# Kernel optimization log

Measured on AMD Instinct MI355X. Metric: run time of the kernel, lower is better.

The kernel has to match this reference:

```python
import jax, jax.numpy as jnp
import numpy as np

NUM_HEADS = 16
DIM = 1024


def setup_inputs() -> dict:
    key = jax.random.key(0)
    k1, k2, k3, k4 = jax.random.split(key, 4)
    B, N, C = 4, 2048, DIM
    x = jax.random.normal(k1, (B, N, C), dtype=jnp.float32)
    # weights stored in apply orientation: y = x @ W (+ b)
    W_qkv = jax.random.normal(k2, (C, 3 * C), dtype=jnp.float32) * (C ** -0.5)
    W_out = jax.random.normal(k3, (C, C), dtype=jnp.float32) * (C ** -0.5)
    b_out = jax.random.normal(k4, (C,), dtype=jnp.float32) * 0.01
    return {"hidden_states": x, "W_qkv": W_qkv, "W_out": W_out, "b_out": b_out}


def reference(hidden_states, W_qkv, W_out, b_out):
    B, N, C = hidden_states.shape
    H = NUM_HEADS
    Dh = C // H
    scale = Dh ** -0.5
    qkv = hidden_states @ W_qkv                      # [B, N, 3C]
    qkv = qkv.reshape(B, N, 3, H, Dh).transpose(2, 0, 3, 1, 4)  # [3, B, H, N, Dh]
    q, k, v = qkv[0], qkv[1], qkv[2]
    scores = jnp.einsum('bhnd,bhmd->bhnm', q, k) * scale  # [B, H, N, N]
    probs = jax.nn.softmax(scores, axis=-1)
    out = jnp.einsum('bhnm,bhmd->bhnd', probs, v)    # [B, H, N, Dh]
    out = out.transpose(0, 2, 1, 3).reshape(B, N, C)  # merge heads
    return out @ W_out + b_out                        # dropout p=0 -> identity
```

## Files before the change

kernel.cpp:

```cpp
#include <hip/hip_runtime.h>
#include <hip/hip_bf16.h>
#include <stdint.h>

#define BATCH 4
#define SEQN  2048
#define DIMC  1024
#define NHEADS 16
#define DHEAD 64
#define BH_TOT 64
#define MROWS 8192

typedef __attribute__((ext_vector_type(8))) short bf16x8;
typedef __attribute__((ext_vector_type(4))) float f32x4;

__device__ __forceinline__ unsigned short bf16_rtne(float f){
  union { float f; unsigned u; } v; v.f = f;
  unsigned u = v.u;
  return (unsigned short)((u + 0x7FFFu + ((u >> 16) & 1u)) >> 16);
}
__device__ __forceinline__ float bf16f(unsigned short h){
  union { unsigned u; float f; } v; v.u = ((unsigned)h) << 16;
  return v.f;
}
__device__ __forceinline__ unsigned cvt_pk_bf16(float lo, float hi){
  unsigned r;
  asm("v_cvt_pk_bf16_f32 %0, %1, %2" : "=v"(r) : "v"(lo), "v"(hi));
  return r;
}

__device__ __forceinline__ void async16(void* lds, const void* g){
  __builtin_amdgcn_global_load_lds((const __attribute__((address_space(1))) void*)g,
                                   (__attribute__((address_space(3))) void*)lds, 16, 0, 0);
}

__global__ __launch_bounds__(256) void split_rows_k(const float* __restrict__ X,
    unsigned short* __restrict__ O, int nrows, int Kc){
  int q4 = Kc >> 2;
  int total = nrows * q4;
  int idx = blockIdx.x*256 + threadIdx.x;
  if (idx >= total) return;
  int row = idx / q4, c = idx - row*q4;
  const float4 v = *(const float4*)(X + ((size_t)row*Kc + c*4));
  float fv[4] = {v.x, v.y, v.z, v.w};
  unsigned short hi[4], lo[4];
#pragma unroll
  for (int j=0;j<4;j++){ hi[j] = bf16_rtne(fv[j]); lo[j] = bf16_rtne(fv[j] - bf16f(hi[j])); }
  size_t ob = (size_t)row*(2*Kc) + c*4;
  ushort4 h; h.x=hi[0]; h.y=hi[1]; h.z=hi[2]; h.w=hi[3];
  ushort4 l2; l2.x=lo[0]; l2.y=lo[1]; l2.z=lo[2]; l2.w=lo[3];
  *(ushort4*)(O + ob) = h;
  *(ushort4*)(O + ob + Kc) = l2;
}

__global__ __launch_bounds__(256) void transpose_split_k(const float* __restrict__ W,
    unsigned short* __restrict__ Wt, int K, int Nc){
  __shared__ float tile[32][33];
  int tx = threadIdx.x & 31, ty = threadIdx.x >> 5;
  int n0 = blockIdx.x*32, k0 = blockIdx.y*32;
#pragma unroll
  for (int i=0;i<4;i++){
    int k = k0 + ty + i*8;
    tile[ty + i*8][tx] = W[(size_t)k*Nc + n0 + tx];
  }
  __syncthreads();
#pragma unroll
  for (int i=0;i<4;i++){
    int n = n0 + ty + i*8;
    float f = tile[tx][ty + i*8];
    unsigned short hi = bf16_rtne(f);
    unsigned short lo = bf16_rtne(f - bf16f(hi));
    Wt[(size_t)n*(2*K) + k0 + tx] = hi;
    Wt[(size_t)n*(2*K) + K + k0 + tx] = lo;
  }
}

__global__ __launch_bounds__(256) void gemm_split_k(
    const unsigned short* __restrict__ A, const unsigned short* __restrict__ Bt,
    float* __restrict__ C, const float* __restrict__ bias, int M, int Nc, int K)
{
  __shared__ unsigned short a_lds[2][4096];
  __shared__ unsigned short b_lds[2][4096];
  const int t = threadIdx.x, w = t>>6, l = t&63, lg = l>>4, ll = l&15;
  const int wr = w>>1, wc = w&1;
  const int nbx = gridDim.x;
  const int nwg = nbx * gridDim.y;
  const int orig = blockIdx.y*nbx + blockIdx.x;
  const int id = ((orig & 7) * (nwg >> 3)) + (orig >> 3);
  const int m0 = (id % nbx)*128, n0 = (id / nbx)*128;
  const int ldk = 2*K;
  const int nkt = (3*K) >> 5;
  f32x4 acc[4][4];
#pragma unroll
  for (int m=0;m<4;m++)
#pragma unroll
    for (int n=0;n<4;n++) acc[m][n] = (f32x4){0.f,0.f,0.f,0.f};

  auto stage = [&](int buf, int kt){
    int kp = kt*32;
    int ac = (kp < K)   ? kp : kp - K;
    int bc = (kp < 2*K) ? kp : kp - 2*K;
#pragma unroll
    for (int i=0;i<2;i++){
      int s = t + i*256; int row = s>>2; int sl = s&3; int sl2 = sl ^ (row&3);
      async16(&a_lds[buf][s*8], A + (size_t)(m0+row)*ldk + ac + sl2*8);
    }
#pragma unroll
    for (int i=0;i<2;i++){
      int s = t + i*256; int row = s>>2; int sl = s&3; int sl2 = sl ^ (row&3);
      async16(&b_lds[buf][s*8], Bt + (size_t)(n0+row)*ldk + bc + sl2*8);
    }
  };

  stage(0, 0);
  __syncthreads();
  for (int kt=0; kt<nkt; ++kt){
    int cur = kt&1;
    if (kt+1 < nkt) stage(cur^1, kt+1);
    bf16x8 af[4], bfr[4];
#pragma unroll
    for (int m=0;m<4;m++){
      int row = wr*64 + m*16 + ll;
      af[m] = *(const bf16x8*)&a_lds[cur][row*32 + ((lg ^ (row&3))*8)];
    }
#pragma unroll
    for (int n=0;n<4;n++){
      int row = wc*64 + n*16 + ll;
      bfr[n] = *(const bf16x8*)&b_lds[cur][row*32 + ((lg ^ (row&3))*8)];
    }
#pragma unroll
    for (int m=0;m<4;m++)
#pragma unroll
      for (int n=0;n<4;n++)
        acc[m][n] = __builtin_amdgcn_mfma_f32_16x16x32_bf16(af[m], bfr[n], acc[m][n], 0,0,0);
    __syncthreads();
  }
#pragma unroll
  for (int m=0;m<4;m++)
#pragma unroll
    for (int n=0;n<4;n++){
      int col = n0 + wc*64 + n*16 + ll;
      float bv = bias ? bias[col] : 0.f;
#pragma unroll
      for (int r=0;r<4;r++){
        int row = m0 + wr*64 + m*16 + lg*4 + r;
        C[(size_t)row*Nc + col] = acc[m][n][r] + bv;
      }
    }
}

#define QSCALE 0.18033688f
__global__ __launch_bounds__(256) void split_qk_k(const float* __restrict__ qkv,
    unsigned short* __restrict__ Qo, unsigned short* __restrict__ Ko){
  int idx = blockIdx.x*256 + threadIdx.x;
  int d4 = idx & 15, n = (idx>>4) & (SEQN-1), bh = idx >> 15;
  int b = bh>>4, h = bh&15;
  size_t base = ((size_t)(b*SEQN + n))*3072 + h*64 + d4*4;
  float4 q = *(const float4*)(qkv + base);
  float4 k = *(const float4*)(qkv + base + 1024);
  float fq[4] = {q.x*QSCALE, q.y*QSCALE, q.z*QSCALE, q.w*QSCALE};
  float fk[4] = {k.x, k.y, k.z, k.w};
  unsigned short qh[4], ql[4], kh[4];
#pragma unroll
  for (int j=0;j<4;j++){
    qh[j] = bf16_rtne(fq[j]); ql[j] = bf16_rtne(fq[j] - bf16f(qh[j]));
    kh[j] = bf16_rtne(fk[j]);
  }
  size_t obq = ((size_t)bh*SEQN + n)*128 + d4*4;
  size_t obk = ((size_t)bh*SEQN + n)*64 + d4*4;
  ushort4 u;
  u.x=qh[0];u.y=qh[1];u.z=qh[2];u.w=qh[3]; *(ushort4*)(Qo+obq) = u;
  u.x=ql[0];u.y=ql[1];u.z=ql[2];u.w=ql[3]; *(ushort4*)(Qo+obq+64) = u;
  u.x=kh[0];u.y=kh[1];u.z=kh[2];u.w=kh[3]; *(ushort4*)(Ko+obk) = u;
}

__global__ __launch_bounds__(256) void build_vt_k(const float* __restrict__ qkv,
    unsigned short* __restrict__ Vt){
  __shared__ float tile[64][65];
  const int mt = blockIdx.x, bh = blockIdx.y;
  const int b = bh>>4, h = bh&15;
  const int t = threadIdx.x;
  const int r = t>>2, seg = t&3;
  size_t src = ((size_t)(b*SEQN + mt*64 + r))*3072 + 2048 + h*64 + seg*16;
#pragma unroll
  for (int j=0;j<4;j++){
    float4 v = *(const float4*)(qkv + src + j*4);
    tile[r][seg*16 + j*4 + 0] = v.x;
    tile[r][seg*16 + j*4 + 1] = v.y;
    tile[r][seg*16 + j*4 + 2] = v.z;
    tile[r][seg*16 + j*4 + 3] = v.w;
  }
  __syncthreads();
  const int d = r, ms = seg;
  unsigned short o16[16];
#pragma unroll
  for (int j=0;j<16;j++) o16[j] = bf16_rtne(tile[ms*16 + j][d]);
  size_t dst = ((size_t)(bh*64 + d))*SEQN + mt*64 + ms*16;
  uint4 u0, u1;
  unsigned* pu = (unsigned*)&u0;
  unsigned* pv = (unsigned*)&u1;
#pragma unroll
  for (int j=0;j<4;j++){
    pu[j] = (unsigned)o16[2*j]   | ((unsigned)o16[2*j+1]<<16);
    pv[j] = (unsigned)o16[8+2*j] | ((unsigned)o16[9+2*j]<<16);
  }
  *(uint4*)(Vt + dst) = u0;
  *(uint4*)(Vt + dst + 8) = u1;
}

__global__ __launch_bounds__(256, 4) void attn_k(const unsigned short* __restrict__ Q,
    const unsigned short* __restrict__ Kh, const unsigned short* __restrict__ Vt,
    float* __restrict__ att)
{
  __shared__ unsigned short k_lds[2][4096];
  __shared__ unsigned short v_lds[2][4096];
  __shared__ unsigned p_lds[4][512];
  const int orig = blockIdx.y*gridDim.x + blockIdx.x;
  const int id = ((orig & 7) << 8) + (orig >> 3);
  const int qt = id & 31, bh = id >> 5;
  const int b = bh>>4, h = bh&15;
  const int t = threadIdx.x, w = t>>6, l = t&63, lg = l>>4, ll = l&15;
  const size_t kvbase = (size_t)bh*SEQN;

  bf16x8 qf[4];
  {
    size_t qrow = (kvbase + qt*64 + w*16 + ll) * 128;
#pragma unroll
    for (int i=0;i<4;i++)
      qf[i] = *(const bf16x8*)(Q + qrow + i*32 + lg*8);
  }
  f32x4 o[4];
#pragma unroll
  for (int d=0; d<4; d++) o[d] = (f32x4){0.f,0.f,0.f,0.f};
  float lsum = 0.f;

  auto stage = [&](int buf, int kv){
    int m0 = kv*64;
#pragma unroll
    for (int i=0;i<2;i++){
      int s = t + i*256; int row = s>>3; int sl = s&7; int sl2 = sl ^ (row&7);
      async16(&k_lds[buf][s*8], Kh + (kvbase + m0 + row)*64 + sl2*8);
    }
#pragma unroll
    for (int i=0;i<2;i++){
      int s = t + i*256; int row = s>>3; int sl = s&7; int sl2 = sl ^ (row&7);
      async16(&v_lds[buf][s*8], Vt + ((size_t)bh*64 + row)*SEQN + m0 + sl2*8);
    }
  };

  stage(0, 0);
  __syncthreads();
  const int NKV = SEQN/64;
  for (int kv=0; kv<NKV; ++kv){
    int cur = kv&1;
    if (kv+1 < NKV) stage(cur^1, kv+1);
#pragma unroll
    for (int nt=0; nt<4; ++nt){
      int row = nt*16 + ll;
      bf16x8 kf0 = *(const bf16x8*)&k_lds[cur][row*64 + (((0*4+lg) ^ (row&7))*8)];
      bf16x8 kf1 = *(const bf16x8*)&k_lds[cur][row*64 + (((1*4+lg) ^ (row&7))*8)];
      f32x4 a = (f32x4){0.f,0.f,0.f,0.f};
      __builtin_amdgcn_s_setprio(1);
      a = __builtin_amdgcn_mfma_f32_16x16x32_bf16(kf0, qf[0], a, 0,0,0);
      a = __builtin_amdgcn_mfma_f32_16x16x32_bf16(kf1, qf[1], a, 0,0,0);
      a = __builtin_amdgcn_mfma_f32_16x16x32_bf16(kf0, qf[2], a, 0,0,0);
      a = __builtin_amdgcn_mfma_f32_16x16x32_bf16(kf1, qf[3], a, 0,0,0);
      __builtin_amdgcn_s_setprio(0);
      float e0 = exp2f(a[0]), e1 = exp2f(a[1]), e2 = exp2f(a[2]), e3 = exp2f(a[3]);
      lsum += (e0 + e1) + (e2 + e3);
      unsigned pk0 = cvt_pk_bf16(e0, e1);
      unsigned pk1 = cvt_pk_bf16(e2, e3);
      int c0 = nt*8 + lg*2;
      int addr = ll*32 + (((c0>>2) ^ (ll&7))<<2) + (c0&3);
      *(uint2*)&p_lds[w][addr] = make_uint2(pk0, pk1);
    }
#pragma unroll
    for (int ks=0; ks<2; ++ks){
      int chunk = ks*4 + lg;
      bf16x8 pf = *(const bf16x8*)&p_lds[w][ll*32 + ((chunk ^ (ll&7))<<2)];
      __builtin_amdgcn_s_setprio(1);
#pragma unroll
      for (int dt=0; dt<4; ++dt){
        int row = dt*16 + ll;
        bf16x8 vf = *(const bf16x8*)&v_lds[cur][row*64 + (((ks*4+lg) ^ (row&7))*8)];
        o[dt] = __builtin_amdgcn_mfma_f32_16x16x32_bf16(pf, vf, o[dt], 0,0,0);
      }
      __builtin_amdgcn_s_setprio(0);
    }
    __syncthreads();
  }
  float tot = lsum;
  tot += __shfl_xor(tot, 16);
  tot += __shfl_xor(tot, 32);
  float inv = 1.0f / tot;
#pragma unroll
  for (int r=0;r<4;r++){
    float rl = __shfl(inv, lg*4 + r);
    int qrow = qt*64 + w*16 + lg*4 + r;
    size_t ob = ((size_t)(b*SEQN + qrow))*DIMC + h*64;
#pragma unroll
    for (int dt=0; dt<4; ++dt)
      att[ob + dt*16 + ll] = o[dt][r] * rl;
  }
}

extern "C" void kernel_launch(void* const* d_in, const int* in_sizes, int n_in,
                              void* d_out, int out_size, void* d_ws, size_t ws_size,
                              hipStream_t stream){
  const float* x    = (const float*)d_in[0];
  const float* Wqkv = (const float*)d_in[1];
  const float* Wout = (const float*)d_in[2];
  const float* bout = (const float*)d_in[3];
  float* out = (float*)d_out;

  char* ws = (char*)d_ws;
  size_t off = 0;
  auto walloc = [&](size_t bytes) -> void* {
    void* p = ws + off; off += (bytes + 255) & ~(size_t)255; return p;
  };
  unsigned short* x_hl   = (unsigned short*)walloc((size_t)MROWS*2048*2);
  unsigned short* wqkv_t = (unsigned short*)walloc((size_t)3072*2048*2);
  float*          qkv    = (float*)walloc((size_t)MROWS*3072*4);
  unsigned short* q_hl   = (unsigned short*)walloc((size_t)BH_TOT*SEQN*128*2);
  unsigned short* k_h    = (unsigned short*)walloc((size_t)BH_TOT*SEQN*64*2);
  unsigned short* vt     = (unsigned short*)walloc((size_t)BH_TOT*64*SEQN*2);
  unsigned short* wout_t = (unsigned short*)walloc((size_t)1024*2048*2);
  float*          att    = qkv;
  unsigned short* att_hl = x_hl;

  split_rows_k<<<8192, 256, 0, stream>>>(x, x_hl, MROWS, DIMC);
  transpose_split_k<<<dim3(3072/32, 1024/32), 256, 0, stream>>>(Wqkv, wqkv_t, 1024, 3072);
  transpose_split_k<<<dim3(1024/32, 1024/32), 256, 0, stream>>>(Wout, wout_t, 1024, 1024);
  gemm_split_k<<<dim3(MROWS/128, 3072/128), 256, 0, stream>>>(x_hl, wqkv_t, qkv, nullptr, MROWS, 3072, 1024);
  split_qk_k<<<(BH_TOT*SEQN*16)/256, 256, 0, stream>>>(qkv, q_hl, k_h);
  build_vt_k<<<dim3(SEQN/64, BH_TOT), 256, 0, stream>>>(qkv, vt);
  attn_k<<<dim3(SEQN/64, BH_TOT), 256, 0, stream>>>(q_hl, k_h, vt, att);
  split_rows_k<<<8192, 256, 0, stream>>>(att, att_hl, MROWS, DIMC);
  gemm_split_k<<<dim3(MROWS/128, 1024/128), 256, 0, stream>>>(att_hl, wout_t, out, bout, MROWS, 1024, 1024);
}
```

Baseline: 545.8 us.

## Deepen GEMM k-tile pipeline with fragment-ordered LDS and fuse attention output split

The split-bf16 GEMM now stages 64-wide k tiles as two 32-wide halves stored in MFMA fragment order, so no XOR swizzle is needed. Each half is double-buffered and loaded with explicit vmcnt waits and raw barriers, and the next tile's loads are issued right after the LDS reads so they overlap the MFMAs. The launch moves to a 1D grid with 2 blocks per CU. Separately, the attention kernel writes the hi/lo bf16 split of its output directly, which removes the fp32 intermediate and the extra split_rows pass before the output projection. The cost is double the LDS use per block and fragile hand-written wait counts.

```diff
diff --git a/kernel.cpp b/kernel.cpp
--- a/kernel.cpp
+++ b/kernel.cpp
@@ -74,76 +74,107 @@
   }
 }
 
-__global__ __launch_bounds__(256) void gemm_split_k(
+__global__ __launch_bounds__(256, 2) void gemm_split_k(
     const unsigned short* __restrict__ A, const unsigned short* __restrict__ Bt,
     float* __restrict__ C, const float* __restrict__ bias, int M, int Nc, int K)
 {
-  __shared__ unsigned short a_lds[2][4096];
-  __shared__ unsigned short b_lds[2][4096];
+  __shared__ unsigned short a_lds[2][2][4096];
+  __shared__ unsigned short b_lds[2][2][4096];
   const int t = threadIdx.x, w = t>>6, l = t&63, lg = l>>4, ll = l&15;
   const int wr = w>>1, wc = w&1;
-  const int nbx = gridDim.x;
-  const int nwg = nbx * gridDim.y;
-  const int orig = blockIdx.y*nbx + blockIdx.x;
-  const int id = ((orig & 7) * (nwg >> 3)) + (orig >> 3);
-  const int m0 = (id % nbx)*128, n0 = (id / nbx)*128;
+  const int nbm = M>>7;
+  const int nwg = nbm*(Nc>>7);
+  const int orig = blockIdx.x;
+  const int id = ((orig&7)*(nwg>>3)) + (orig>>3);
+  const int m0 = (id & (nbm-1))<<7, n0 = (id/nbm)<<7;
   const int ldk = 2*K;
-  const int nkt = (3*K) >> 5;
+  const int nkt = (3*K)>>6;
   f32x4 acc[4][4];
 #pragma unroll
   for (int m=0;m<4;m++)
 #pragma unroll
     for (int n=0;n<4;n++) acc[m][n] = (f32x4){0.f,0.f,0.f,0.f};
 
-  auto stage = [&](int buf, int kt){
-    int kp = kt*32;
-    int ac = (kp < K)   ? kp : kp - K;
-    int bc = (kp < 2*K) ? kp : kp - 2*K;
+  auto stage = [&](int d, int kk, int kt){
+    const int kp = kt<<6;
+    const int ac = (kp <   K) ? kp : kp -   K;
+    const int bc = (kp < 2*K) ? kp : kp - 2*K;
 #pragma unroll
     for (int i=0;i<2;i++){
-      int s = t + i*256; int row = s>>2; int sl = s&3; int sl2 = sl ^ (row&3);
-      async16(&a_lds[buf][s*8], A + (size_t)(m0+row)*ldk + ac + sl2*8);
+      int F = i*4 + w;
+      async16(&a_lds[d][kk][(i*256+t)*8],
+              A + (size_t)(m0 + F*16 + ll)*ldk + ac + kk*32 + lg*8);
     }
 #pragma unroll
     for (int i=0;i<2;i++){
-      int s = t + i*256; int row = s>>2; int sl = s&3; int sl2 = sl ^ (row&3);
-      async16(&b_lds[buf][s*8], Bt + (size_t)(n0+row)*ldk + bc + sl2*8);
+      int F = i*4 + w;
+      async16(&b_lds[d][kk][(i*256+t)*8],
+              Bt + (size_t)(n0 + F*16 + ll)*ldk + bc + kk*32 + lg*8);
     }
   };
 
-  stage(0, 0);
-  __syncthreads();
-  for (int kt=0; kt<nkt; ++kt){
-    int cur = kt&1;
-    if (kt+1 < nkt) stage(cur^1, kt+1);
-    bf16x8 af[4], bfr[4];
-#pragma unroll
-    for (int m=0;m<4;m++){
-      int row = wr*64 + m*16 + ll;
-      af[m] = *(const bf16x8*)&a_lds[cur][row*32 + ((lg ^ (row&3))*8)];
-    }
-#pragma unroll
-    for (int n=0;n<4;n++){
-      int row = wc*64 + n*16 + ll;
-      bfr[n] = *(const bf16x8*)&b_lds[cur][row*32 + ((lg ^ (row&3))*8)];
-    }
-#pragma unroll
-    for (int m=0;m<4;m++)
-#pragma unroll
-      for (int n=0;n<4;n++)
-        acc[m][n] = __builtin_amdgcn_mfma_f32_16x16x32_bf16(af[m], bfr[n], acc[m][n], 0,0,0);
-    __syncthreads();
-  }
-#pragma unroll
-  for (int m=0;m<4;m++)
-#pragma unroll
-    for (int n=0;n<4;n++){
-      int col = n0 + wc*64 + n*16 + ll;
+  stage(0, 0, 0);
+  stage(0, 1, 0);
+
+  for (int kt=0; kt<nkt-1; ++kt){
+    const int d = kt&1;
+#pragma unroll
+    for (int kk=0; kk<2; ++kk){
+      asm volatile("s_waitcnt vmcnt(4)" ::: "memory");
+      __builtin_amdgcn_s_barrier();
+      __builtin_amdgcn_sched_barrier(0);
+      bf16x8 af[4], bfr[4];
+#pragma unroll
+      for (int fm=0;fm<4;fm++)
+        af[fm] = *(const bf16x8*)&a_lds[d][kk][(wr*4+fm)*512 + l*8];
+#pragma unroll
+      for (int fn=0;fn<4;fn++)
+        bfr[fn] = *(const bf16x8*)&b_lds[d][kk][(wc*4+fn)*512 + l*8];
+      stage(d^1, kk, kt+1);
+      __builtin_amdgcn_s_setprio(1);
+#pragma unroll
+      for (int fm=0;fm<4;fm++)
+#pragma unroll
+        for (int fn=0;fn<4;fn++)
+          acc[fm][fn] = __builtin_amdgcn_mfma_f32_16x16x32_bf16(af[fm], bfr[fn], acc[fm][fn], 0,0,0);
+      __builtin_amdgcn_s_setprio(0);
+    }
+  }
+  {
+    const int d = (nkt-1)&1;
+#pragma unroll
+    for (int kk=0; kk<2; ++kk){
+      if (kk==0) asm volatile("s_waitcnt vmcnt(4)" ::: "memory");
+      else       asm volatile("s_waitcnt vmcnt(0)" ::: "memory");
+      __builtin_amdgcn_s_barrier();
+      __builtin_amdgcn_sched_barrier(0);
+      bf16x8 af[4], bfr[4];
+#pragma unroll
+      for (int fm=0;fm<4;fm++)
+        af[fm] = *(const bf16x8*)&a_lds[d][kk][(wr*4+fm)*512 + l*8];
+#pragma unroll
+      for (int fn=0;fn<4;fn++)
+        bfr[fn] = *(const bf16x8*)&b_lds[d][kk][(wc*4+fn)*512 + l*8];
+      __builtin_amdgcn_s_setprio(1);
+#pragma unroll
+      for (int fm=0;fm<4;fm++)
+#pragma unroll
+        for (int fn=0;fn<4;fn++)
+          acc[fm][fn] = __builtin_amdgcn_mfma_f32_16x16x32_bf16(af[fm], bfr[fn], acc[fm][fn], 0,0,0);
+      __builtin_amdgcn_s_setprio(0);
+    }
+  }
+
+#pragma unroll
+  for (int fm=0;fm<4;fm++)
+#pragma unroll
+    for (int fn=0;fn<4;fn++){
+      int col = n0 + wc*64 + fn*16 + ll;
       float bv = bias ? bias[col] : 0.f;
 #pragma unroll
       for (int r=0;r<4;r++){
-        int row = m0 + wr*64 + m*16 + lg*4 + r;
-        C[(size_t)row*Nc + col] = acc[m][n][r] + bv;
+        int row = m0 + wr*64 + fm*16 + lg*4 + r;
+        C[(size_t)row*Nc + col] = acc[fm][fn][r] + bv;
       }
     }
 }
@@ -209,7 +240,7 @@
 
 __global__ __launch_bounds__(256, 4) void attn_k(const unsigned short* __restrict__ Q,
     const unsigned short* __restrict__ Kh, const unsigned short* __restrict__ Vt,
-    float* __restrict__ att)
+    unsigned short* __restrict__ att_hl)
 {
   __shared__ unsigned short k_lds[2][4096];
   __shared__ unsigned short v_lds[2][4096];
@@ -296,10 +327,15 @@
   for (int r=0;r<4;r++){
     float rl = __shfl(inv, lg*4 + r);
     int qrow = qt*64 + w*16 + lg*4 + r;
-    size_t ob = ((size_t)(b*SEQN + qrow))*DIMC + h*64;
-#pragma unroll
-    for (int dt=0; dt<4; ++dt)
-      att[ob + dt*16 + ll] = o[dt][r] * rl;
+    size_t ob = ((size_t)(b*SEQN + qrow))*2048 + h*64;
+#pragma unroll
+    for (int dt=0; dt<4; ++dt){
+      float f = o[dt][r] * rl;
+      unsigned short hi = bf16_rtne(f);
+      unsigned short lo = bf16_rtne(f - bf16f(hi));
+      att_hl[ob + dt*16 + ll] = hi;
+      att_hl[ob + 1024 + dt*16 + ll] = lo;
+    }
   }
 }
 
@@ -324,16 +360,14 @@
   unsigned short* k_h    = (unsigned short*)walloc((size_t)BH_TOT*SEQN*64*2);
   unsigned short* vt     = (unsigned short*)walloc((size_t)BH_TOT*64*SEQN*2);
   unsigned short* wout_t = (unsigned short*)walloc((size_t)1024*2048*2);
-  float*          att    = qkv;
   unsigned short* att_hl = x_hl;
 
   split_rows_k<<<8192, 256, 0, stream>>>(x, x_hl, MROWS, DIMC);
   transpose_split_k<<<dim3(3072/32, 1024/32), 256, 0, stream>>>(Wqkv, wqkv_t, 1024, 3072);
   transpose_split_k<<<dim3(1024/32, 1024/32), 256, 0, stream>>>(Wout, wout_t, 1024, 1024);
-  gemm_split_k<<<dim3(MROWS/128, 3072/128), 256, 0, stream>>>(x_hl, wqkv_t, qkv, nullptr, MROWS, 3072, 1024);
+  gemm_split_k<<<1536, 256, 0, stream>>>(x_hl, wqkv_t, qkv, nullptr, MROWS, 3072, 1024);
   split_qk_k<<<(BH_TOT*SEQN*16)/256, 256, 0, stream>>>(qkv, q_hl, k_h);
   build_vt_k<<<dim3(SEQN/64, BH_TOT), 256, 0, stream>>>(qkv, vt);
-  attn_k<<<dim3(SEQN/64, BH_TOT), 256, 0, stream>>>(q_hl, k_h, vt, att);
-  split_rows_k<<<8192, 256, 0, stream>>>(att, att_hl, MROWS, DIMC);
-  gemm_split_k<<<dim3(MROWS/128, 1024/128), 256, 0, stream>>>(att_hl, wout_t, out, bout, MROWS, 1024, 1024);
-}
+  attn_k<<<dim3(SEQN/64, BH_TOT), 256, 0, stream>>>(q_hl, k_h, vt, att_hl);
+  gemm_split_k<<<512, 256, 0, stream>>>(att_hl, wout_t, out, bout, MROWS, 1024, 1024);
+}
```

After: 629.3 us. 1.15x slower.

## Retile split-bf16 GEMM to 256x128 with triple-buffered LDS; fuse att split

Applied to the files above, without the earlier changes.

The split-bf16 GEMM moves to 512-thread blocks computing 256x128 tiles. It gains a three-stage LDS ring with raw vmcnt waits and one barrier per k-step, MFMA-friendly pre-permuted LDS layout, and setprio around the MFMA loop. The attention kernel now writes the hi/lo bf16 split of its output directly, removing the fp32 att buffer round trip and the separate split_rows launch. Risks are the larger LDS footprint limiting occupancy and correctness depending on the hand-written vmcnt counts.

```diff
diff --git a/kernel.cpp b/kernel.cpp
--- a/kernel.cpp
+++ b/kernel.cpp
@@ -74,76 +74,81 @@
   }
 }
 
-__global__ __launch_bounds__(256) void gemm_split_k(
+__global__ __launch_bounds__(512, 4) void gemm_split_k(
     const unsigned short* __restrict__ A, const unsigned short* __restrict__ Bt,
     float* __restrict__ C, const float* __restrict__ bias, int M, int Nc, int K)
 {
-  __shared__ unsigned short a_lds[2][4096];
-  __shared__ unsigned short b_lds[2][4096];
-  const int t = threadIdx.x, w = t>>6, l = t&63, lg = l>>4, ll = l&15;
-  const int wr = w>>1, wc = w&1;
-  const int nbx = gridDim.x;
-  const int nwg = nbx * gridDim.y;
-  const int orig = blockIdx.y*nbx + blockIdx.x;
-  const int id = ((orig & 7) * (nwg >> 3)) + (orig >> 3);
-  const int m0 = (id % nbx)*128, n0 = (id / nbx)*128;
+  __shared__ unsigned short a_lds[3*8192];
+  __shared__ unsigned short b_lds[3*4096];
+  const int t = threadIdx.x, wid = t>>6, l = t&63, lg = l>>4, ll = l&15;
+  const int wm = wid>>1, wn = wid&1;
+  const int nbm = M>>8;
+  const int nwg = nbm*(Nc>>7);
+  const int orig = blockIdx.x;
+  const int id = ((orig&7)*(nwg>>3)) + (orig>>3);
+  const int m0 = (id % nbm)<<8, n0 = (id / nbm)<<7;
   const int ldk = 2*K;
-  const int nkt = (3*K) >> 5;
+  const int nkt = (3*K)>>5;
   f32x4 acc[4][4];
 #pragma unroll
-  for (int m=0;m<4;m++)
-#pragma unroll
-    for (int n=0;n<4;n++) acc[m][n] = (f32x4){0.f,0.f,0.f,0.f};
-
-  auto stage = [&](int buf, int kt){
-    int kp = kt*32;
-    int ac = (kp < K)   ? kp : kp - K;
-    int bc = (kp < 2*K) ? kp : kp - 2*K;
+  for (int i=0;i<4;i++)
+#pragma unroll
+    for (int j=0;j<4;j++) acc[i][j] = (f32x4){0.f,0.f,0.f,0.f};
+
+  auto stageA = [&](int wb, int kt2){
+    const int kp = kt2<<5;
+    const int ac = (kp < K) ? kp : kp - K;
 #pragma unroll
     for (int i=0;i<2;i++){
-      int s = t + i*256; int row = s>>2; int sl = s&3; int sl2 = sl ^ (row&3);
-      async16(&a_lds[buf][s*8], A + (size_t)(m0+row)*ldk + ac + sl2*8);
-    }
-#pragma unroll
-    for (int i=0;i<2;i++){
-      int s = t + i*256; int row = s>>2; int sl = s&3; int sl2 = sl ^ (row&3);
-      async16(&b_lds[buf][s*8], Bt + (size_t)(n0+row)*ldk + bc + sl2*8);
+      int b = i*8 + wid;
+      async16(&a_lds[wb*8192 + b*512 + l*8],
+              A + (size_t)(m0 + b*16 + ll)*ldk + ac + lg*8);
     }
   };
-
-  stage(0, 0);
-  __syncthreads();
+  auto stageB = [&](int wb, int kt2){
+    const int kp = kt2<<5;
+    const int bc = (kp < 2*K) ? kp : kp - 2*K;
+    async16(&b_lds[wb*4096 + wid*512 + l*8],
+            Bt + (size_t)(n0 + wid*16 + ll)*ldk + bc + lg*8);
+  };
+
+  stageA(0, 0); stageB(0, 0);
+  stageA(1, 1); stageB(1, 1);
+
   for (int kt=0; kt<nkt; ++kt){
-    int cur = kt&1;
-    if (kt+1 < nkt) stage(cur^1, kt+1);
-    bf16x8 af[4], bfr[4];
-#pragma unroll
-    for (int m=0;m<4;m++){
-      int row = wr*64 + m*16 + ll;
-      af[m] = *(const bf16x8*)&a_lds[cur][row*32 + ((lg ^ (row&3))*8)];
-    }
-#pragma unroll
-    for (int n=0;n<4;n++){
-      int row = wc*64 + n*16 + ll;
-      bfr[n] = *(const bf16x8*)&b_lds[cur][row*32 + ((lg ^ (row&3))*8)];
-    }
-#pragma unroll
-    for (int m=0;m<4;m++)
-#pragma unroll
-      for (int n=0;n<4;n++)
-        acc[m][n] = __builtin_amdgcn_mfma_f32_16x16x32_bf16(af[m], bfr[n], acc[m][n], 0,0,0);
-    __syncthreads();
-  }
-#pragma unroll
-  for (int m=0;m<4;m++)
-#pragma unroll
-    for (int n=0;n<4;n++){
-      int col = n0 + wc*64 + n*16 + ll;
+    if (kt < nkt-1) asm volatile("s_waitcnt vmcnt(3)\n\ts_barrier" ::: "memory");
+    else            asm volatile("s_waitcnt vmcnt(0)\n\ts_barrier" ::: "memory");
+    const int rb = kt % 3;
+    const unsigned short* ab = &a_lds[rb*8192];
+    const unsigned short* bb = &b_lds[rb*4096];
+    bf16x8 af[4], bf[4];
+#pragma unroll
+    for (int i=0;i<4;i++) af[i] = *(const bf16x8*)&ab[(wm*4+i)*512 + l*8];
+#pragma unroll
+    for (int j=0;j<4;j++) bf[j] = *(const bf16x8*)&bb[(wn*4+j)*512 + l*8];
+    if (kt+2 < nkt){
+      const int wb = (kt+2) % 3;
+      stageA(wb, kt+2); stageB(wb, kt+2);
+    }
+    __builtin_amdgcn_s_setprio(1);
+#pragma unroll
+    for (int i=0;i<4;i++)
+#pragma unroll
+      for (int j=0;j<4;j++)
+        acc[i][j] = __builtin_amdgcn_mfma_f32_16x16x32_bf16(af[i], bf[j], acc[i][j], 0,0,0);
+    __builtin_amdgcn_s_setprio(0);
+  }
+
+#pragma unroll
+  for (int i=0;i<4;i++)
+#pragma unroll
+    for (int j=0;j<4;j++){
+      int col = n0 + wn*64 + j*16 + ll;
       float bv = bias ? bias[col] : 0.f;
 #pragma unroll
       for (int r=0;r<4;r++){
-        int row = m0 + wr*64 + m*16 + lg*4 + r;
-        C[(size_t)row*Nc + col] = acc[m][n][r] + bv;
+        int row = m0 + wm*64 + i*16 + lg*4 + r;
+        C[(size_t)row*Nc + col] = acc[i][j][r] + bv;
       }
     }
 }
@@ -209,7 +214,7 @@
 
 __global__ __launch_bounds__(256, 4) void attn_k(const unsigned short* __restrict__ Q,
     const unsigned short* __restrict__ Kh, const unsigned short* __restrict__ Vt,
-    float* __restrict__ att)
+    unsigned short* __restrict__ att_hl)
 {
   __shared__ unsigned short k_lds[2][4096];
   __shared__ unsigned short v_lds[2][4096];
@@ -296,10 +301,15 @@
   for (int r=0;r<4;r++){
     float rl = __shfl(inv, lg*4 + r);
     int qrow = qt*64 + w*16 + lg*4 + r;
-    size_t ob = ((size_t)(b*SEQN + qrow))*DIMC + h*64;
-#pragma unroll
-    for (int dt=0; dt<4; ++dt)
-      att[ob + dt*16 + ll] = o[dt][r] * rl;
+    size_t ob = ((size_t)(b*SEQN + qrow))*2048 + h*64;
+#pragma unroll
+    for (int dt=0; dt<4; ++dt){
+      float f = o[dt][r] * rl;
+      unsigned short hi = bf16_rtne(f);
+      unsigned short lo = bf16_rtne(f - bf16f(hi));
+      att_hl[ob + dt*16 + ll] = hi;
+      att_hl[ob + 1024 + dt*16 + ll] = lo;
+    }
   }
 }
 
@@ -324,16 +334,14 @@
   unsigned short* k_h    = (unsigned short*)walloc((size_t)BH_TOT*SEQN*64*2);
   unsigned short* vt     = (unsigned short*)walloc((size_t)BH_TOT*64*SEQN*2);
   unsigned short* wout_t = (unsigned short*)walloc((size_t)1024*2048*2);
-  float*          att    = qkv;
   unsigned short* att_hl = x_hl;
 
   split_rows_k<<<8192, 256, 0, stream>>>(x, x_hl, MROWS, DIMC);
   transpose_split_k<<<dim3(3072/32, 1024/32), 256, 0, stream>>>(Wqkv, wqkv_t, 1024, 3072);
   transpose_split_k<<<dim3(1024/32, 1024/32), 256, 0, stream>>>(Wout, wout_t, 1024, 1024);
-  gemm_split_k<<<dim3(MROWS/128, 3072/128), 256, 0, stream>>>(x_hl, wqkv_t, qkv, nullptr, MROWS, 3072, 1024);
+  gemm_split_k<<<768, 512, 0, stream>>>(x_hl, wqkv_t, qkv, nullptr, MROWS, 3072, 1024);
   split_qk_k<<<(BH_TOT*SEQN*16)/256, 256, 0, stream>>>(qkv, q_hl, k_h);
   build_vt_k<<<dim3(SEQN/64, BH_TOT), 256, 0, stream>>>(qkv, vt);
-  attn_k<<<dim3(SEQN/64, BH_TOT), 256, 0, stream>>>(q_hl, k_h, vt, att);
-  split_rows_k<<<8192, 256, 0, stream>>>(att, att_hl, MROWS, DIMC);
-  gemm_split_k<<<dim3(MROWS/128, 1024/128), 256, 0, stream>>>(att_hl, wout_t, out, bout, MROWS, 1024, 1024);
-}
+  attn_k<<<dim3(SEQN/64, BH_TOT), 256, 0, stream>>>(q_hl, k_h, vt, att_hl);
+  gemm_split_k<<<256, 512, 0, stream>>>(att_hl, wout_t, out, bout, MROWS, 1024, 1024);
+}
```

New measurement: 559.5 us. 2.5% more time.
